# Kernel optimization log

Hardware: AMD Instinct MI355X
Metric: run time of the kernel (lower is better)

Reference implementation:

```python
import jax, jax.numpy as jnp
import numpy as np

X_GRID, Y_GRID = 192, 132
HW = X_GRID * Y_GRID            # 25344
NUM_PROP = 500
NUM_CLS = 6
RADIUS = 10
L_WIN = (2 * RADIUS + 1) ** 2   # 441
D = 128
N_HEADS = 8
D_HEAD = D // N_HEADS
VX, VY = 0.64, 0.64             # feature_map_stride * voxel_size
PC_X0, PC_Y0 = -61.44, -42.24


def _bev_pos():
    # create_2D_grid: linspace(0, size-1, size) + 0.5, meshgrid 'ij', flatten row-major
    bx, by = jnp.meshgrid(jnp.arange(X_GRID, dtype=jnp.float32) + 0.5,
                          jnp.arange(Y_GRID, dtype=jnp.float32) + 0.5, indexing='ij')
    return jnp.stack([bx.reshape(-1), by.reshape(-1)], axis=-1)[None]  # [1, HW, 2]


def conv2d(x, w, b):
    y = jax.lax.conv_general_dilated(x, w, (1, 1), 'SAME',
                                     dimension_numbers=('NCHW', 'OIHW', 'NCHW'))
    return y + b[None, :, None, None]


def maxpool3_valid(x):
    return jax.lax.reduce_window(x, -jnp.inf, jax.lax.max,
                                 (1, 1, 3, 3), (1, 1, 1, 1), 'VALID')


def layer_norm(x, g, b, eps=1e-5):
    m = jnp.mean(x, axis=-1, keepdims=True)
    v = jnp.var(x, axis=-1, keepdims=True)
    return (x - m) * jax.lax.rsqrt(v + eps) * g + b


def pos_emb(p, W1, b1, W2, b2):
    return jax.nn.relu(p @ W1 + b1) @ W2 + b2


def _forward(inputs, W_shared, b_shared, W_hm, b_hm, W_cls, b_cls,
             W_pos1, b_pos1, W_pos2, b_pos2, Wq, bq, Wk, bk, Wv, bv, Wo, bo,
             ln1_g, ln1_b, ln2_g, ln2_b, W_ff1, b_ff1, W_ff2, b_ff2,
             W_center, b_center, W_height, b_height, W_dim, b_dim,
             W_rot, b_rot, W_iou, b_iou, W_hm2, b_hm2):
    x = jnp.transpose(inputs, (0, 1, 3, 2))          # [B,C,192,132]
    B = x.shape[0]
    lidar_feat = jax.nn.relu(conv2d(x, W_shared, b_shared))   # [B,128,192,132]
    lff = lidar_feat.reshape(B, D, HW)

    dense_heatmap = conv2d(lidar_feat, W_hm, b_hm)            # [B,6,192,132]
    heatmap = jax.nn.sigmoid(jax.lax.stop_gradient(dense_heatmap))  # detached in original

    # local-max NMS: 3x3 maxpool on inner region, zeros at border; classes 3..5 bypass NMS
    inner = maxpool3_valid(heatmap)
    local_max = jnp.pad(inner, ((0, 0), (0, 0), (1, 1), (1, 1)))
    local_max = local_max.at[:, 3:6].set(heatmap[:, 3:6])
    hm = heatmap * (heatmap == local_max)

    # threshold + top-k proposals (replaces nonzero+pad+MySortImpe plugin)
    hm_flat = hm.reshape(B, NUM_CLS * HW)
    vals = jnp.where(hm_flat > 0.01, hm_flat, 0.0)
    _, top = jax.lax.top_k(vals, NUM_PROP)            # [B,500]
    cls = top // HW
    sp = top % HW

    query_feat = jnp.take_along_axis(lff, sp[:, None, :], axis=2)  # [B,128,500]
    oh = jax.nn.one_hot(cls, NUM_CLS, dtype=lff.dtype)             # [B,500,6]
    query_feat = query_feat + jnp.einsum('bpc,oc->bop', oh, W_cls) + b_cls[None, :, None]

    bev_pos = jnp.broadcast_to(_bev_pos(), (B, HW, 2))
    query_pos = jnp.take_along_axis(bev_pos, sp[:, :, None], axis=1)  # [B,500,2]

    # windowed key indices (faithful to original //x_grid, %y_grid arithmetic)
    rng = jnp.arange(-RADIUS, RADIUS + 1)
    rx, ry = jnp.meshgrid(rng, rng, indexing='ij')
    kx = (sp // X_GRID)[:, :, None, None] + rx[None, None]
    ky = (sp % Y_GRID)[:, :, None, None] + ry[None, None]
    key_idx = kx.reshape(B, NUM_PROP, L_WIN) * X_GRID + ky.reshape(B, NUM_PROP, L_WIN)
    key_mask = (key_idx < 0) | (key_idx >= HW)
    key_idx = jnp.clip(key_idx, 0, HW - 1)

    key_feat = jnp.take_along_axis(lff, key_idx.reshape(B, 1, -1), axis=2)
    key_feat = key_feat.reshape(B, D, NUM_PROP, L_WIN)
    key_pos = jnp.take_along_axis(bev_pos, key_idx.reshape(B, -1, 1), axis=1)
    key_pos = key_pos.reshape(B, NUM_PROP, L_WIN, 2)

    # decoder: cross-attention of each proposal over its 441-key window
    N = B * NUM_PROP
    q = query_feat.transpose(0, 2, 1).reshape(N, D)
    k = key_feat.transpose(0, 2, 3, 1).reshape(N, L_WIN, D)
    mask = key_mask.reshape(N, L_WIN)
    qpe = pos_emb(query_pos.reshape(N, 2), W_pos1, b_pos1, W_pos2, b_pos2)
    kpe = pos_emb(key_pos.reshape(N, L_WIN, 2), W_pos1, b_pos1, W_pos2, b_pos2)

    qh = ((q + qpe) @ Wq + bq).reshape(N, N_HEADS, D_HEAD)
    kh = ((k + kpe) @ Wk + bk).reshape(N, L_WIN, N_HEADS, D_HEAD)
    vh = (k @ Wv + bv).reshape(N, L_WIN, N_HEADS, D_HEAD)
    scores = jnp.einsum('nhd,nlhd->nhl', qh, kh) / np.float32(np.sqrt(D_HEAD))
    scores = jnp.where(mask[:, None, :], jnp.float32(-1e9), scores)
    attn = jax.nn.softmax(scores, axis=-1)
    ctx = jnp.einsum('nhl,nlhd->nhd', attn, vh).reshape(N, D)
    x1 = layer_norm(q + ctx @ Wo + bo, ln1_g, ln1_b)
    ff = jax.nn.relu(x1 @ W_ff1 + b_ff1) @ W_ff2 + b_ff2
    x2 = layer_norm(x1 + ff, ln2_g, ln2_b)

    qf = x2.reshape(B, NUM_PROP, D).transpose(0, 2, 1)   # [B,128,500]
    head = lambda W, b: jnp.einsum('bcp,oc->bop', qf, W) + b[None, :, None]
    center = head(W_center, b_center) + query_pos.transpose(0, 2, 1)
    height = head(W_height, b_height)
    dim = head(W_dim, b_dim)
    rot = head(W_rot, b_rot)
    iou = head(W_iou, b_iou)
    hm2 = head(W_hm2, b_hm2)

    # get_bboxes / decode_bbox
    score = jax.nn.sigmoid(hm2)                          # [B,6,500]
    _ = (iou + 1.0) * 0.5                                # computed, unused (as in original)
    final_preds = jnp.argmax(score, axis=1).astype(score.dtype)
    final_scores = jnp.max(score, axis=1)
    cx = center[:, 0:1] * VX + PC_X0
    cy = center[:, 1:2] * VY + PC_Y0
    dim = jnp.exp(dim)
    height = height - dim[:, 2:3] * 0.5
    rot = jnp.arctan(rot[:, 0:1] / (rot[:, 1:2] + 1e-6))
    box = jnp.concatenate([cx, cy, height, dim, rot,
                           final_preds[:, None, :], final_scores[:, None, :]], axis=1)
    return box.transpose(0, 2, 1)                        # [B,500,9]


def setup_inputs() -> dict:
    key = jax.random.key(0)
    ks = jax.random.split(key, 20)
    r = lambda k, shape, s=0.02: jax.random.normal(k, shape, dtype=jnp.float32) * s
    z = lambda n: jnp.zeros((n,), dtype=jnp.float32)
    o = lambda n: jnp.ones((n,), dtype=jnp.float32)
    return {
        'inputs': jax.random.normal(ks[0], (1, 256, 132, 192), dtype=jnp.float32),
        'W_shared': r(ks[1], (128, 256, 3, 3)), 'b_shared': z(128),
        'W_hm': r(ks[2], (6, 128, 3, 3)), 'b_hm': z(6),
        'W_cls': r(ks[3], (128, 6)), 'b_cls': z(128),
        'W_pos1': r(ks[4], (2, 128)), 'b_pos1': z(128),
        'W_pos2': r(ks[5], (128, 128)), 'b_pos2': z(128),
        'Wq': r(ks[6], (128, 128)), 'bq': z(128),
        'Wk': r(ks[7], (128, 128)), 'bk': z(128),
        'Wv': r(ks[8], (128, 128)), 'bv': z(128),
        'Wo': r(ks[9], (128, 128)), 'bo': z(128),
        'ln1_g': o(128), 'ln1_b': z(128),
        'ln2_g': o(128), 'ln2_b': z(128),
        'W_ff1': r(ks[10], (128, 256)), 'b_ff1': z(256),
        'W_ff2': r(ks[11], (256, 128)), 'b_ff2': z(128),
        'W_center': r(ks[12], (2, 128)), 'b_center': z(2),
        'W_height': r(ks[13], (1, 128)), 'b_height': z(1),
        'W_dim': r(ks[14], (3, 128)), 'b_dim': z(3),
        'W_rot': r(ks[15], (2, 128)), 'b_rot': z(2),
        'W_iou': r(ks[16], (1, 128)), 'b_iou': z(1),
        'W_hm2': r(ks[17], (6, 128)), 'b_hm2': z(6),
    }


def reference(inputs, W_shared, b_shared, W_hm, b_hm, W_cls, b_cls,
              W_pos1, b_pos1, W_pos2, b_pos2, Wq, bq, Wk, bk, Wv, bv, Wo, bo,
              ln1_g, ln1_b, ln2_g, ln2_b, W_ff1, b_ff1, W_ff2, b_ff2,
              W_center, b_center, W_height, b_height, W_dim, b_dim,
              W_rot, b_rot, W_iou, b_iou, W_hm2, b_hm2):
    return _forward(inputs, W_shared, b_shared, W_hm, b_hm, W_cls, b_cls,
                    W_pos1, b_pos1, W_pos2, b_pos2, Wq, bq, Wk, bk, Wv, bv, Wo, bo,
                    ln1_g, ln1_b, ln2_g, ln2_b, W_ff1, b_ff1, W_ff2, b_ff2,
                    W_center, b_center, W_height, b_height, W_dim, b_dim,
                    W_rot, b_rot, W_iou, b_iou, W_hm2, b_hm2)
```

## Files before the change

### kernel.cpp

```cpp
#include <hip/hip_runtime.h>
#include <math.h>
#include <float.h>

#define XG 192
#define YG 132
#define HW 25344
#define NCLS 6
#define NPROP 500
#define LWIN 441
#define CAP 2048

typedef unsigned short ushort_t;
typedef __attribute__((ext_vector_type(8))) short bf8v;
typedef __attribute__((ext_vector_type(4))) float f4v;

static __device__ __forceinline__ int imin(int a,int b){return a<b?a:b;}
static __device__ __forceinline__ int imax(int a,int b){return a>b?a:b;}

__device__ __forceinline__ void gl_lds16(const float* gp, float* lp){
  __builtin_amdgcn_global_load_lds(
      (const __attribute__((address_space(1))) unsigned int*)gp,
      (__attribute__((address_space(3))) unsigned int*)lp,
      16, 0, 0);
}
__device__ __forceinline__ void gl_lds16u(const ushort_t* gp, ushort_t* lp){
  __builtin_amdgcn_global_load_lds(
      (const __attribute__((address_space(1))) unsigned int*)gp,
      (__attribute__((address_space(3))) unsigned int*)lp,
      16, 0, 0);
}

__device__ __forceinline__ ushort_t f2bf(float x){
  unsigned u = __float_as_uint(x);
  return (ushort_t)((u + 0x7FFFu + ((u>>16)&1u)) >> 16);
}
__device__ __forceinline__ float bf2f(ushort_t h){
  return __uint_as_float(((unsigned)h)<<16);
}

__global__ __launch_bounds__(256) void k_wt(const float* __restrict__ Ws,
                                            const float* __restrict__ Whm,
                                            const float* __restrict__ Wq,
                                            const float* __restrict__ Wp2,
                                            const float* __restrict__ Wo,
                                            const float* __restrict__ Wf1,
                                            const float* __restrict__ Wf2,
                                            float* __restrict__ W6,
                                            float* __restrict__ WQT,
                                            float* __restrict__ WP2T,
                                            float* __restrict__ WOT,
                                            float* __restrict__ WF1T,
                                            float* __restrict__ WF2T,
                                            ushort_t* __restrict__ BQ0,
                                            ushort_t* __restrict__ BQ1,
                                            ushort_t* __restrict__ BQ2,
                                            int* __restrict__ Z){
  int t = blockIdx.x*256 + threadIdx.x;
  if (t < 294912){
    int kl = t & 31;
    int rest = t >> 5;
    int n = rest & 127;
    int tc = rest >> 7;
    int tap = tc >> 3, chunk = tc & 7;
    int c = chunk*32 + kl;
    float v = Ws[(size_t)n*2304 + c*9 + tap];
    ushort_t h0 = f2bf(v);
    float r1 = v - bf2f(h0);
    ushort_t h1 = f2bf(r1);
    float r2 = r1 - bf2f(h1);
    ushort_t h2 = f2bf(r2);
    size_t dst = (size_t)tc*5120 + n*40 + kl;
    BQ0[dst] = h0; BQ1[dst] = h1; BQ2[dst] = h2;
  }
  if (t < 6912){
    int c = t & 127, row = t >> 7;
    int cls = row / 9, tap = row % 9;
    W6[t] = Whm[(size_t)cls*1152 + c*9 + tap];
  }
  if (t < 16384){
    int k = t & 127, c = t >> 7;
    WQT[t]  = Wq [(size_t)k*128 + c];
    WP2T[t] = Wp2[(size_t)k*128 + c];
    WOT[t]  = Wo [(size_t)k*128 + c];
  }
  if (t < 32768){
    { int k = t & 127, o = t >> 7;  WF1T[t] = Wf1[(size_t)k*256 + o]; }
    { int k = t & 255, c = t >> 8;  WF2T[t] = Wf2[(size_t)k*128 + c]; }
  }
  if (t < 65568) Z[t] = 0;
}

__global__ __launch_bounds__(256, 3) void k_conv1(const float* __restrict__ IN,
                                                  const ushort_t* __restrict__ BQ0,
                                                  const ushort_t* __restrict__ BQ1,
                                                  const ushort_t* __restrict__ BQ2,
                                                  const float* __restrict__ bias,
                                                  float* __restrict__ LFF){
  const int b  = blockIdx.x;
  const int i0 = (b % 3) * 64;
  const int j  = b / 3;
  const int tid = threadIdx.x;
  const int w    = tid >> 6;
  const int lane = tid & 63;
  const int l15  = lane & 15, quad = lane >> 4;
  __shared__ __align__(16) ushort_t SM[23280];
  ushort_t* As0 = SM;
  ushort_t* As1 = SM + 2640;
  ushort_t* As2 = SM + 5280;
  ushort_t* Bs0 = SM + 7920;
  ushort_t* Bs1 = SM + 13040;
  ushort_t* Bs2 = SM + 18160;
  f4v acc[4][2];
  #pragma unroll
  for (int mq=0;mq<4;++mq)
    #pragma unroll
    for (int nt=0;nt<2;++nt) acc[mq][nt] = (f4v){0.f,0.f,0.f,0.f};

  for (int chunk=0; chunk<8; ++chunk){
    for (int kw=0; kw<3; ++kw){
      __syncthreads();
      {
        int gj = j - 1 + kw;
        bool jok = (unsigned)gj < 132u;
        for (int e = tid; e < 2112; e += 256){
          int c = e / 66, ii = e - c*66;
          int gi = i0 - 1 + ii;
          float v = 0.f;
          if (jok && (unsigned)gi < 192u)
            v = IN[(size_t)(chunk*32 + c)*25344 + gj*192 + gi];
          ushort_t h0 = f2bf(v);
          float r1 = v - bf2f(h0);
          ushort_t h1 = f2bf(r1);
          float r2 = r1 - bf2f(h1);
          ushort_t h2 = f2bf(r2);
          int a = ii*40 + c;
          As0[a] = h0; As1[a] = h1; As2[a] = h2;
        }
      }
      for (int kh=0; kh<3; ++kh){
        if (kh > 0) __syncthreads();
        {
          int tc = (kh*3 + kw)*8 + chunk;
          const ushort_t* s0 = BQ0 + (size_t)tc*5120;
          const ushort_t* s1 = BQ1 + (size_t)tc*5120;
          const ushort_t* s2 = BQ2 + (size_t)tc*5120;
          gl_lds16u(s0 + (size_t)tid*8,       Bs0 + (size_t)(w*64)*8);
          gl_lds16u(s0 + (size_t)(256+tid)*8, Bs0 + (size_t)(256 + w*64)*8);
          gl_lds16u(s1 + (size_t)tid*8,       Bs1 + (size_t)(w*64)*8);
          gl_lds16u(s1 + (size_t)(256+tid)*8, Bs1 + (size_t)(256 + w*64)*8);
          gl_lds16u(s2 + (size_t)tid*8,       Bs2 + (size_t)(w*64)*8);
          gl_lds16u(s2 + (size_t)(256+tid)*8, Bs2 + (size_t)(256 + w*64)*8);
          if (tid < 128){
            gl_lds16u(s0 + (size_t)(512+tid)*8, Bs0 + (size_t)(512 + w*64)*8);
            gl_lds16u(s1 + (size_t)(512+tid)*8, Bs1 + (size_t)(512 + w*64)*8);
            gl_lds16u(s2 + (size_t)(512+tid)*8, Bs2 + (size_t)(512 + w*64)*8);
          }
        }
        __syncthreads();
        bf8v A0[4], A1[4], A2[4];
        #pragma unroll
        for (int mq=0; mq<4; ++mq){
          int off = (mq*16 + l15 + kh)*40 + quad*8;
          A0[mq] = *(const bf8v*)&As0[off];
          A1[mq] = *(const bf8v*)&As1[off];
          A2[mq] = *(const bf8v*)&As2[off];
        }
        bf8v B0[2], B1[2], B2[2];
        #pragma unroll
        for (int ntl=0; ntl<2; ++ntl){
          int off = ((w*2+ntl)*16 + l15)*40 + quad*8;
          B0[ntl] = *(const bf8v*)&Bs0[off];
          B1[ntl] = *(const bf8v*)&Bs1[off];
          B2[ntl] = *(const bf8v*)&Bs2[off];
        }
        #pragma unroll
        for (int mq=0;mq<4;++mq){
          #pragma unroll
          for (int ntl=0;ntl<2;++ntl){
            f4v c = acc[mq][ntl];
            c = __builtin_amdgcn_mfma_f32_16x16x32_bf16(A0[mq], B0[ntl], c, 0,0,0);
            c = __builtin_amdgcn_mfma_f32_16x16x32_bf16(A0[mq], B1[ntl], c, 0,0,0);
            c = __builtin_amdgcn_mfma_f32_16x16x32_bf16(A1[mq], B0[ntl], c, 0,0,0);
            c = __builtin_amdgcn_mfma_f32_16x16x32_bf16(A0[mq], B2[ntl], c, 0,0,0);
            c = __builtin_amdgcn_mfma_f32_16x16x32_bf16(A1[mq], B1[ntl], c, 0,0,0);
            c = __builtin_amdgcn_mfma_f32_16x16x32_bf16(A2[mq], B0[ntl], c, 0,0,0);
            acc[mq][ntl] = c;
          }
        }
      }
    }
  }
  __syncthreads();
  float* Cs = (float*)SM;
  #pragma unroll
  for (int mq=0;mq<4;++mq)
    #pragma unroll
    for (int ntl=0;ntl<2;++ntl)
      #pragma unroll
      for (int r=0;r<4;++r){
        int m = mq*16 + quad*4 + r;
        int oc = (w*2+ntl)*16 + l15;
        Cs[m*128 + oc] = acc[mq][ntl][r];
      }
  __syncthreads();
  for (int e = tid; e < 2048; e += 256){
    int m = e >> 5, ocq = e & 31;
    float4 v = *(float4*)&Cs[m*128 + ocq*4];
    float4 bs = *(const float4*)&bias[ocq*4];
    v.x = fmaxf(v.x + bs.x, 0.f);
    v.y = fmaxf(v.y + bs.y, 0.f);
    v.z = fmaxf(v.z + bs.z, 0.f);
    v.w = fmaxf(v.w + bs.w, 0.f);
    int p = (i0 + m)*132 + j;
    *(float4*)&LFF[(size_t)p*128 + ocq*4] = v;
  }
}

__global__ __launch_bounds__(256) void k_mid(const float* __restrict__ LFF,
                                             const float* __restrict__ W1, const float* __restrict__ b1,
                                             const float* __restrict__ W2, const float* __restrict__ b2,
                                             const float* __restrict__ Wk, const float* __restrict__ bk,
                                             const float* __restrict__ Wv, const float* __restrict__ bv,
                                             float* __restrict__ KK, float* __restrict__ VV,
                                             const float* __restrict__ W6, const float* __restrict__ bhm,
                                             float* __restrict__ HMS){
  __shared__ float smem[12288];
  const int tid = threadIdx.x;
  const int wv4 = tid >> 6;
  if (blockIdx.x < 792){
    float* hs   = smem;
    float* sf   = smem + 4096;
    float* wbuf = smem + 8192;
    const int p0 = blockIdx.x*32;
    for (int e=tid; e<4096; e+=256){
      int k = e>>5, px = e&31;
      int p = p0+px;
      float bx = (float)(p/132)+0.5f, by = (float)(p%132)+0.5f;
      hs[k*32+px] = fmaxf(bx*W1[k] + by*W1[128+k] + b1[k], 0.f);
    }
    for (int e=tid; e<4096; e+=256){
      int px = e>>7, k = e&127;
      sf[k*32+px] = LFF[(size_t)(p0+px)*128 + k];
    }
    const int pxg = tid & 15, ocg = tid >> 4;
    const int px0 = pxg*2, oc0 = ocg*8;
    float accA[2][8];
    #pragma unroll
    for (int r=0;r<2;++r)
      #pragma unroll
      for (int u=0;u<8;++u) accA[r][u]=0.f;
    for (int c0=0; c0<128; c0+=32){
      __syncthreads();
      const float* wsrc = W2 + (size_t)c0*128;
      #pragma unroll
      for (int r=0;r<4;++r)
        gl_lds16(wsrc + (size_t)(r*256+tid)*4, wbuf + (size_t)(r*256+wv4*64)*4);
      __syncthreads();
      #pragma unroll 2
      for (int k=0;k<32;++k){
        float a0 = hs[(c0+k)*32+px0], a1 = hs[(c0+k)*32+px0+1];
        const float4* w = (const float4*)(wbuf + (size_t)k*128 + oc0);
        float4 w0 = w[0], w1 = w[1];
        accA[0][0]+=a0*w0.x; accA[0][1]+=a0*w0.y; accA[0][2]+=a0*w0.z; accA[0][3]+=a0*w0.w;
        accA[0][4]+=a0*w1.x; accA[0][5]+=a0*w1.y; accA[0][6]+=a0*w1.z; accA[0][7]+=a0*w1.w;
        accA[1][0]+=a1*w0.x; accA[1][1]+=a1*w0.y; accA[1][2]+=a1*w0.z; accA[1][3]+=a1*w0.w;
        accA[1][4]+=a1*w1.x; accA[1][5]+=a1*w1.y; accA[1][6]+=a1*w1.z; accA[1][7]+=a1*w1.w;
      }
    }
    __syncthreads();
    #pragma unroll
    for (int u=0;u<8;++u){
      float bb = b2[oc0+u];
      hs[(oc0+u)*32+px0]   = sf[(oc0+u)*32+px0]   + accA[0][u] + bb;
      hs[(oc0+u)*32+px0+1] = sf[(oc0+u)*32+px0+1] + accA[1][u] + bb;
    }
    float accK[2][8], accV[2][8];
    #pragma unroll
    for (int u=0;u<8;++u){
      float k0 = bk[oc0+u], v0 = bv[oc0+u];
      accK[0][u]=k0; accK[1][u]=k0; accV[0][u]=v0; accV[1][u]=v0;
    }
    for (int c0=0; c0<128; c0+=16){
      __syncthreads();
      #pragma unroll
      for (int r=0;r<2;++r){
        gl_lds16(Wk + (size_t)c0*128 + (size_t)(r*256+tid)*4, wbuf + (size_t)(r*256+wv4*64)*4);
        gl_lds16(Wv + (size_t)c0*128 + (size_t)(r*256+tid)*4, wbuf + 2048 + (size_t)(r*256+wv4*64)*4);
      }
      __syncthreads();
      #pragma unroll 2
      for (int k=0;k<16;++k){
        int kk = c0+k;
        float s0 = hs[kk*32+px0], s1 = hs[kk*32+px0+1];
        float f0 = sf[kk*32+px0], f1 = sf[kk*32+px0+1];
        const float4* wkp = (const float4*)(wbuf + (size_t)k*128 + oc0);
        const float4* wvp = (const float4*)(wbuf + 2048 + (size_t)k*128 + oc0);
        float4 k0v = wkp[0], k1v = wkp[1], v0v = wvp[0], v1v = wvp[1];
        accK[0][0]+=s0*k0v.x; accK[0][1]+=s0*k0v.y; accK[0][2]+=s0*k0v.z; accK[0][3]+=s0*k0v.w;
        accK[0][4]+=s0*k1v.x; accK[0][5]+=s0*k1v.y; accK[0][6]+=s0*k1v.z; accK[0][7]+=s0*k1v.w;
        accK[1][0]+=s1*k0v.x; accK[1][1]+=s1*k0v.y; accK[1][2]+=s1*k0v.z; accK[1][3]+=s1*k0v.w;
        accK[1][4]+=s1*k1v.x; accK[1][5]+=s1*k1v.y; accK[1][6]+=s1*k1v.z; accK[1][7]+=s1*k1v.w;
        accV[0][0]+=f0*v0v.x; accV[0][1]+=f0*v0v.y; accV[0][2]+=f0*v0v.z; accV[0][3]+=f0*v0v.w;
        accV[0][4]+=f0*v1v.x; accV[0][5]+=f0*v1v.y; accV[0][6]+=f0*v1v.z; accV[0][7]+=f0*v1v.w;
        accV[1][0]+=f1*v0v.x; accV[1][1]+=f1*v0v.y; accV[1][2]+=f1*v0v.z; accV[1][3]+=f1*v0v.w;
        accV[1][4]+=f1*v1v.x; accV[1][5]+=f1*v1v.y; accV[1][6]+=f1*v1v.z; accV[1][7]+=f1*v1v.w;
      }
    }
    #pragma unroll
    for (int r=0;r<2;++r){
      int p = p0+px0+r;
      float4* oK = (float4*)(KK + (size_t)p*128 + oc0);
      float4* oV = (float4*)(VV + (size_t)p*128 + oc0);
      float4 t0, t1;
      t0.x=accK[r][0]; t0.y=accK[r][1]; t0.z=accK[r][2]; t0.w=accK[r][3];
      t1.x=accK[r][4]; t1.y=accK[r][5]; t1.z=accK[r][6]; t1.w=accK[r][7];
      oK[0]=t0; oK[1]=t1;
      t0.x=accV[r][0]; t0.y=accV[r][1]; t0.z=accV[r][2]; t0.w=accV[r][3];
      t1.x=accV[r][4]; t1.y=accV[r][5]; t1.z=accV[r][6]; t1.w=accV[r][7];
      oV[0]=t0; oV[1]=t1;
    }
  } else {
    float* w6s = smem;
    float* red = smem + 8192;
    for (int e=tid; e<6912; e+=256) w6s[e] = W6[e];
    __syncthreads();
    int lane = tid & 63, wave = tid >> 6;
    int p = (blockIdx.x - 792)*64 + lane;
    int i = p/132, j = p%132;
    float acc[6] = {0.f,0.f,0.f,0.f,0.f,0.f};
    int cbase = wave*32;
    #pragma unroll
    for (int kh=0; kh<3; ++kh){
      int gi = i+kh-1;
      if ((unsigned)gi >= 192u) continue;
      #pragma unroll
      for (int kw=0; kw<3; ++kw){
        int gj = j+kw-1;
        if ((unsigned)gj >= 132u) continue;
        const float* row = LFF + (size_t)(gi*132+gj)*128 + cbase;
        int tap = kh*3+kw;
        #pragma unroll
        for (int cq=0; cq<8; ++cq){
          float4 v = *(const float4*)(row + cq*4);
          #pragma unroll
          for (int cls=0; cls<6; ++cls){
            float4 wv = *(const float4*)(w6s + (size_t)(cls*9+tap)*128 + cbase + cq*4);
            acc[cls] += v.x*wv.x + v.y*wv.y + v.z*wv.z + v.w*wv.w;
          }
        }
      }
    }
    __syncthreads();
    #pragma unroll
    for (int c=0;c<6;++c) red[(wave*6+c)*64 + lane] = acc[c];
    __syncthreads();
    if (wave==0){
      #pragma unroll
      for (int c=0;c<6;++c){
        float s = red[c*64+lane] + red[(6+c)*64+lane] + red[(12+c)*64+lane] + red[(18+c)*64+lane] + bhm[c];
        HMS[(size_t)c*HW + p] = 1.f/(1.f+expf(-s));
      }
    }
  }
}

__global__ __launch_bounds__(256) void k_nms(const float* __restrict__ HMS,
                                             float* __restrict__ VALS,
                                             int* __restrict__ HIST){
  int t = blockIdx.x*256 + threadIdx.x;
  int c = t / HW, p = t % HW;
  int i = p/132, j = p%132;
  float h = HMS[t];
  float v;
  if (c < 3){
    v = 0.f;
    if (i>=1 && i<=190 && j>=1 && j<=130){
      float m = -1e30f;
      #pragma unroll
      for (int di=-1;di<=1;++di)
        #pragma unroll
        for (int dj=-1;dj<=1;++dj)
          m = fmaxf(m, HMS[(size_t)c*HW + (i+di)*132 + (j+dj)]);
      if (h == m) v = h;
    }
  } else v = h;
  if (!(v > 0.01f)) v = 0.f;
  VALS[t] = v;
  if (v > 0.f) atomicAdd(HIST + (__float_as_uint(v)>>16), 1);
}

__global__ __launch_bounds__(1024) void k_scan(const int* __restrict__ HIST, int* __restrict__ SCAN){
  __shared__ int part[1024];
  __shared__ int gsel;
  int t = threadIdx.x;
  int s = 0, base = t*64;
  for (int u=0;u<64;++u) s += HIST[base+u];
  part[t] = s;
  __syncthreads();
  for (int off=1; off<1024; off<<=1){
    int add = (t+off < 1024) ? part[t+off] : 0;
    __syncthreads();
    part[t] += add;
    __syncthreads();
  }
  int total = part[0];
  int mineI = part[t];
  int nextI = (t < 1023) ? part[t+1] : 0;
  if (mineI >= NPROP && nextI < NPROP) gsel = t;
  if (t == 0 && total < NPROP) gsel = -1;
  __syncthreads();
  int g = gsel;
  if (g < 0){
    if (t==0){ SCAN[0] = 0; SCAN[1] = total; }
    return;
  }
  int cumG = (g < 1023) ? part[g+1] : 0;
  if (t < 64){
    int x = HIST[g*64 + t];
    #pragma unroll
    for (int off=1; off<64; off<<=1){
      int y = __shfl_down(x, off);
      x += (t + off < 64) ? y : 0;
    }
    int Snext = __shfl_down(x, 1);
    int incl  = cumG + x;
    int nextc = (t==63) ? cumG : cumG + Snext;
    if (incl >= NPROP && nextc < NPROP){
      SCAN[0] = g*64 + t;
      SCAN[1] = nextc;
    }
  }
}

__global__ __launch_bounds__(256) void k_collect(const float* __restrict__ VALS,
                                                 const int* __restrict__ SCAN,
                                                 int* __restrict__ CNT,
                                                 float* __restrict__ CV, int* __restrict__ CI){
  int t = blockIdx.x*256 + threadIdx.x;
  float v = VALS[t];
  int bstar = SCAN[0];
  if (v > 0.f && (int)(__float_as_uint(v)>>16) >= bstar){
    int pos = atomicAdd(CNT, 1);
    if (pos < CAP){ CV[pos] = v; CI[pos] = t; }
  }
}

__global__ __launch_bounds__(1024) void k_sort(const float* __restrict__ CV, const int* __restrict__ CI,
                                               const int* __restrict__ CNT,
                                               int* __restrict__ TOPS, int* __restrict__ TOPC){
  __shared__ float sv[CAP];
  __shared__ int   si[CAP];
  int tid = threadIdx.x;
  int M = imin(CNT[0], CAP);
  for (int i=tid; i<CAP; i+=1024){
    if (i < M){ sv[i] = CV[i]; si[i] = CI[i]; }
    else      { sv[i] = -1.f;  si[i] = 0x7fffffff; }
  }
  __syncthreads();
  for (int k=2; k<=CAP; k<<=1){
    for (int j=k>>1; j>0; j>>=1){
      for (int i=tid; i<CAP; i+=1024){
        int p = i ^ j;
        if (p > i){
          bool up = ((i & k) == 0);
          float va = sv[i], vb = sv[p];
          int ia = si[i], ib = si[p];
          bool aFirst = (va > vb) || (va == vb && ia < ib);
          bool bFirst = (vb > va) || (vb == va && ib < ia);
          bool doswap = up ? bFirst : aFirst;
          if (doswap){ sv[i]=vb; sv[p]=va; si[i]=ib; si[p]=ia; }
        }
      }
      __syncthreads();
    }
  }
  for (int t=tid; t<NPROP; t+=1024){
    int idx = imin(si[t], NCLS*HW - 1);
    TOPC[t] = idx / HW;
    TOPS[t] = idx % HW;
  }
}

__global__ __launch_bounds__(256) void k_attn(const float* __restrict__ KK, const float* __restrict__ VV,
                                              const float* __restrict__ LFF,
                                              const int* __restrict__ TOPS, const int* __restrict__ TOPC,
                                              const float* __restrict__ Wcls, const float* __restrict__ bcls,
                                              const float* __restrict__ pW1, const float* __restrict__ pb1,
                                              const float* __restrict__ WP2T, const float* __restrict__ pb2,
                                              const float* __restrict__ WQT, const float* __restrict__ bq,
                                              const float* __restrict__ WOT, const float* __restrict__ bo,
                                              const float* __restrict__ g1, const float* __restrict__ b1,
                                              const float* __restrict__ WF1T, const float* __restrict__ bf1,
                                              const float* __restrict__ WF2T, const float* __restrict__ bf2,
                                              const float* __restrict__ g2, const float* __restrict__ b2,
                                              const float* __restrict__ Wc, const float* __restrict__ bc,
                                              const float* __restrict__ Wh, const float* __restrict__ bh,
                                              const float* __restrict__ Wd, const float* __restrict__ bd,
                                              const float* __restrict__ Wr, const float* __restrict__ br,
                                              const float* __restrict__ Whm2, const float* __restrict__ bhm2,
                                              float* __restrict__ out){
  int n = blockIdx.x, tid = threadIdx.x;
  __shared__ __align__(16) float qhL[128];
  __shared__ float sc[8*441];
  __shared__ int   kiL[441];
  __shared__ __align__(16) float ctxL[128];
  __shared__ float xL[128];
  __shared__ float hidL[256];
  __shared__ float sumsL[8];
  __shared__ float stat[2];
  __shared__ float dots[16];
  int sp = TOPS[n];
  int cls = TOPC[n];
  const int kb64 = (tid>>7)*64, c128 = tid&127;
  float qreg = 0.f;
  if (tid < 128){
    float qx = (float)(sp/132)+0.5f, qy = (float)(sp%132)+0.5f;
    ctxL[tid] = fmaxf(qx*pW1[tid] + qy*pW1[128+tid] + pb1[tid], 0.f);
    qreg = LFF[(size_t)sp*128+tid] + Wcls[tid*6+cls] + bcls[tid];
  }
  __syncthreads();
  {
    const float4* wp = (const float4*)(WP2T + (size_t)c128*128 + kb64);
    float pe = 0.f;
    #pragma unroll
    for (int k4=0;k4<16;++k4){
      float4 w = wp[k4]; int kb = kb64 + k4*4;
      pe += ctxL[kb]*w.x + ctxL[kb+1]*w.y + ctxL[kb+2]*w.z + ctxL[kb+3]*w.w;
    }
    sc[tid] = pe;
  }
  __syncthreads();
  if (tid < 128) xL[tid] = qreg + pb2[tid] + sc[tid] + sc[tid+128];
  __syncthreads();
  {
    const float4* wp = (const float4*)(WQT + (size_t)c128*128 + kb64);
    float qh = 0.f;
    #pragma unroll
    for (int k4=0;k4<16;++k4){
      float4 w = wp[k4]; int kb = kb64 + k4*4;
      qh += xL[kb]*w.x + xL[kb+1]*w.y + xL[kb+2]*w.z + xL[kb+3]*w.w;
    }
    sc[tid] = qh;
  }
  __syncthreads();
  if (tid < 128) qhL[tid] = bq[tid] + sc[tid] + sc[tid+128];
  __syncthreads();
  int spx = sp/192, spy = sp%132;
  for (int l = tid; l < 441; l += 256){
    int a = l/21, bb = l%21;
    int kidx = (spx + a - 10)*192 + (spy + bb - 10);
    bool msk = (kidx < 0) || (kidx >= HW);
    int kc = imin(imax(kidx,0), HW-1);
    kiL[l] = kc;
    const float4* kk4 = (const float4*)(KK + (size_t)kc*128);
    const float4* qh4 = (const float4*)qhL;
    #pragma unroll
    for (int hh=0; hh<8; ++hh){
      float acc = 0.f;
      #pragma unroll
      for (int d4=0; d4<4; ++d4){
        float4 kv = kk4[hh*4+d4]; float4 qv = qh4[hh*4+d4];
        acc += kv.x*qv.x + kv.y*qv.y + kv.z*qv.z + kv.w*qv.w;
      }
      sc[hh*441+l] = msk ? -1e9f : acc*0.25f;
    }
  }
  __syncthreads();
  int wave = tid>>6, lane = tid&63;
  for (int hh = wave; hh < 8; hh += 4){
    float mx = -3.0e38f;
    for (int l = lane; l < 441; l += 64) mx = fmaxf(mx, sc[hh*441+l]);
    #pragma unroll
    for (int off=32; off; off>>=1) mx = fmaxf(mx, __shfl_xor(mx, off));
    float sum = 0.f;
    for (int l = lane; l < 441; l += 64){
      float e = __expf(sc[hh*441+l] - mx);
      sc[hh*441+l] = e; sum += e;
    }
    #pragma unroll
    for (int off=32; off; off>>=1) sum += __shfl_xor(sum, off);
    if (lane==0) sumsL[hh] = sum;
  }
  __syncthreads();
  for (int hh = wave; hh < 8; hh += 4){
    float a[16];
    #pragma unroll
    for (int d=0; d<16; ++d) a[d]=0.f;
    for (int l = lane; l < 441; l += 64){
      float w = sc[hh*441+l];
      const float4* vv4 = (const float4*)(VV + (size_t)kiL[l]*128 + hh*16);
      #pragma unroll
      for (int d4=0; d4<4; ++d4){
        float4 v = vv4[d4];
        a[d4*4+0]+=w*v.x; a[d4*4+1]+=w*v.y; a[d4*4+2]+=w*v.z; a[d4*4+3]+=w*v.w;
      }
    }
    #pragma unroll
    for (int d=0; d<16; ++d){
      #pragma unroll
      for (int off=32; off; off>>=1) a[d] += __shfl_xor(a[d], off);
    }
    if (lane==0){
      float inv = 1.f/sumsL[hh];
      #pragma unroll
      for (int d=0; d<16; ++d) ctxL[hh*16+d] = a[d]*inv;
    }
  }
  __syncthreads();
  {
    const float4* wp = (const float4*)(WOT + (size_t)c128*128 + kb64);
    float acc = 0.f;
    #pragma unroll
    for (int k4=0;k4<16;++k4){
      float4 w = wp[k4]; int kb = kb64 + k4*4;
      acc += ctxL[kb]*w.x + ctxL[kb+1]*w.y + ctxL[kb+2]*w.z + ctxL[kb+3]*w.w;
    }
    sc[tid] = acc;
  }
  __syncthreads();
  float x1v = 0.f;
  if (tid < 128){
    x1v = qreg + bo[tid] + sc[tid] + sc[tid+128];
    xL[tid] = x1v;
  }
  __syncthreads();
  if (tid < 64){
    float u0 = xL[tid], u1 = xL[tid+64];
    float s = u0+u1, s2 = u0*u0+u1*u1;
    #pragma unroll
    for (int off=32; off; off>>=1){ s += __shfl_xor(s, off); s2 += __shfl_xor(s2, off); }
    if (tid==0){ float mean = s*(1.f/128.f); float var = s2*(1.f/128.f) - mean*mean;
      stat[0]=mean; stat[1]=rsqrtf(var + 1e-5f); }
  }
  __syncthreads();
  if (tid < 128) xL[tid] = (x1v - stat[0])*stat[1]*g1[tid] + b1[tid];
  __syncthreads();
  {
    const float4* wp = (const float4*)(WF1T + (size_t)tid*128);
    float hv = bf1[tid];
    #pragma unroll 8
    for (int k4=0;k4<32;++k4){
      float4 w = wp[k4]; int kb = k4*4;
      hv += xL[kb]*w.x + xL[kb+1]*w.y + xL[kb+2]*w.z + xL[kb+3]*w.w;
    }
    hidL[tid] = fmaxf(hv, 0.f);
  }
  __syncthreads();
  {
    int kb0 = (tid>>7)*128;
    const float4* wp = (const float4*)(WF2T + (size_t)c128*256 + kb0);
    float acc = 0.f;
    #pragma unroll 8
    for (int k4=0;k4<32;++k4){
      float4 w = wp[k4]; int kb = kb0 + k4*4;
      acc += hidL[kb]*w.x + hidL[kb+1]*w.y + hidL[kb+2]*w.z + hidL[kb+3]*w.w;
    }
    sc[tid] = acc;
  }
  __syncthreads();
  float x2v = 0.f;
  if (tid < 128) x2v = xL[tid] + bf2[tid] + sc[tid] + sc[tid+128];
  __syncthreads();
  if (tid < 128) hidL[tid] = x2v;
  __syncthreads();
  if (tid < 64){
    float u0 = hidL[tid], u1 = hidL[tid+64];
    float s = u0+u1, s2 = u0*u0+u1*u1;
    #pragma unroll
    for (int off=32; off; off>>=1){ s += __shfl_xor(s, off); s2 += __shfl_xor(s2, off); }
    if (tid==0){ float mean = s*(1.f/128.f); float var = s2*(1.f/128.f) - mean*mean;
      stat[0]=mean; stat[1]=rsqrtf(var + 1e-5f); }
  }
  __syncthreads();
  if (tid < 128) xL[tid] = (x2v - stat[0])*stat[1]*g2[tid] + b2[tid];
  __syncthreads();
  if (tid < 14){
    const float* Wp; float bb;
    if (tid < 2)      { Wp = Wc + tid*128;        bb = bc[tid];      }
    else if (tid < 3) { Wp = Wh;                  bb = bh[0];        }
    else if (tid < 6) { Wp = Wd + (tid-3)*128;    bb = bd[tid-3];    }
    else if (tid < 8) { Wp = Wr + (tid-6)*128;    bb = br[tid-6];    }
    else              { Wp = Whm2 + (tid-8)*128;  bb = bhm2[tid-8];  }
    float acc = bb;
    for (int k=0;k<128;++k) acc += xL[k]*Wp[k];
    dots[tid] = acc;
  }
  __syncthreads();
  if (tid == 0){
    float qpx = (float)(sp/132)+0.5f, qpy = (float)(sp%132)+0.5f;
    float cx = (dots[0]+qpx)*0.64f - 61.44f;
    float cy = (dots[1]+qpy)*0.64f - 42.24f;
    float e0 = expf(dots[3]), e1 = expf(dots[4]), e2 = expf(dots[5]);
    float hgt = dots[2] - e2*0.5f;
    float rot = atanf(dots[6]/(dots[7] + 1e-6f));
    float bestv = -1.f; int bestc = 0;
    #pragma unroll
    for (int m=0;m<6;++m){
      float s = 1.f/(1.f + expf(-dots[8+m]));
      if (s > bestv){ bestv = s; bestc = m; }
    }
    float* o = out + (size_t)n*9;
    o[0]=cx; o[1]=cy; o[2]=hgt; o[3]=e0; o[4]=e1; o[5]=e2; o[6]=rot;
    o[7]=(float)bestc; o[8]=bestv;
  }
}

extern "C" void kernel_launch(void* const* d_in, const int* in_sizes, int n_in,
                              void* d_out, int out_size, void* d_ws, size_t ws_size,
                              hipStream_t stream){
  (void)in_sizes; (void)n_in; (void)out_size;
  const float* IN   = (const float*)d_in[0];
  const float* Wsh  = (const float*)d_in[1];
  const float* bsh  = (const float*)d_in[2];
  const float* Whm  = (const float*)d_in[3];
  const float* bhm  = (const float*)d_in[4];
  const float* Wcls = (const float*)d_in[5];
  const float* bcls = (const float*)d_in[6];
  const float* Wp1  = (const float*)d_in[7];
  const float* bp1  = (const float*)d_in[8];
  const float* Wp2  = (const float*)d_in[9];
  const float* bp2  = (const float*)d_in[10];
  const float* Wq   = (const float*)d_in[11];
  const float* bq   = (const float*)d_in[12];
  const float* Wk   = (const float*)d_in[13];
  const float* bk   = (const float*)d_in[14];
  const float* Wv   = (const float*)d_in[15];
  const float* bv   = (const float*)d_in[16];
  const float* Wo   = (const float*)d_in[17];
  const float* bo   = (const float*)d_in[18];
  const float* g1   = (const float*)d_in[19];
  const float* b1   = (const float*)d_in[20];
  const float* g2   = (const float*)d_in[21];
  const float* b2   = (const float*)d_in[22];
  const float* Wf1  = (const float*)d_in[23];
  const float* bf1  = (const float*)d_in[24];
  const float* Wf2  = (const float*)d_in[25];
  const float* bf2  = (const float*)d_in[26];
  const float* Wc   = (const float*)d_in[27];
  const float* bc   = (const float*)d_in[28];
  const float* Wh   = (const float*)d_in[29];
  const float* bh   = (const float*)d_in[30];
  const float* Wd   = (const float*)d_in[31];
  const float* bd   = (const float*)d_in[32];
  const float* Wr   = (const float*)d_in[33];
  const float* br   = (const float*)d_in[34];
  const float* Whm2 = (const float*)d_in[37];
  const float* bhm2 = (const float*)d_in[38];
  float* out = (float*)d_out;
  float* W = (float*)d_ws;

  const size_t N_LFF  = (size_t)HW*128;
  const size_t OFF_LFF  = 0;
  const size_t OFF_KK   = OFF_LFF + N_LFF;
  const size_t OFF_VV   = OFF_KK + N_LFF;
  const size_t OFF_W6   = OFF_VV + N_LFF;
  const size_t OFF_HMS  = OFF_W6 + 6912;
  const size_t OFF_VALS = OFF_HMS + 152064;
  const size_t OFF_HIST = OFF_VALS + 152064;
  const size_t OFF_SCAN = OFF_HIST + 65536;
  const size_t OFF_CNT  = OFF_SCAN + 16;
  const size_t OFF_CV   = OFF_CNT + 16;
  const size_t OFF_CI   = OFF_CV + CAP;
  const size_t OFF_TOPS = OFF_CI + CAP;
  const size_t OFF_TOPC = OFF_TOPS + 512;
  const size_t OFF_WQT  = OFF_TOPC + 512;
  const size_t OFF_WP2T = OFF_WQT + 16384;
  const size_t OFF_WOT  = OFF_WP2T + 16384;
  const size_t OFF_WF1T = OFF_WOT + 16384;
  const size_t OFF_WF2T = OFF_WF1T + 32768;
  const size_t OFF_BQ0  = OFF_WF2T + 32768;
  const size_t OFF_BQ1  = OFF_BQ0 + 184320;
  const size_t OFF_BQ2  = OFF_BQ1 + 184320;
  const size_t TOTAL    = OFF_BQ2 + 184320;
  if (ws_size < TOTAL*sizeof(float)) return;

  ushort_t* BQ0 = (ushort_t*)(W + OFF_BQ0);
  ushort_t* BQ1 = (ushort_t*)(W + OFF_BQ1);
  ushort_t* BQ2 = (ushort_t*)(W + OFF_BQ2);

  k_wt    <<<1152, 256, 0, stream>>>(Wsh, Whm, Wq, Wp2, Wo, Wf1, Wf2,
                                     W+OFF_W6,
                                     W+OFF_WQT, W+OFF_WP2T, W+OFF_WOT, W+OFF_WF1T, W+OFF_WF2T,
                                     BQ0, BQ1, BQ2,
                                     (int*)(W+OFF_HIST));
  k_conv1 <<<396, 256, 0, stream>>>(IN, BQ0, BQ1, BQ2, bsh, W+OFF_LFF);
  k_mid   <<<1188, 256, 0, stream>>>(W+OFF_LFF, Wp1, bp1, Wp2, bp2, Wk, bk, Wv, bv,
                                     W+OFF_KK, W+OFF_VV, W+OFF_W6, bhm, W+OFF_HMS);
  k_nms   <<<594,  256, 0, stream>>>(W+OFF_HMS, W+OFF_VALS, (int*)(W+OFF_HIST));
  k_scan  <<<1,   1024, 0, stream>>>((const int*)(W+OFF_HIST), (int*)(W+OFF_SCAN));
  k_collect<<<594, 256, 0, stream>>>(W+OFF_VALS, (const int*)(W+OFF_SCAN),
                                     (int*)(W+OFF_CNT), W+OFF_CV, (int*)(W+OFF_CI));
  k_sort  <<<1,   1024, 0, stream>>>(W+OFF_CV, (const int*)(W+OFF_CI), (const int*)(W+OFF_CNT),
                                     (int*)(W+OFF_TOPS), (int*)(W+OFF_TOPC));
  k_attn  <<<500,  256, 0, stream>>>(W+OFF_KK, W+OFF_VV, W+OFF_LFF,
                                     (const int*)(W+OFF_TOPS), (const int*)(W+OFF_TOPC),
                                     Wcls, bcls, Wp1, bp1, W+OFF_WP2T, bp2, W+OFF_WQT, bq,
                                     W+OFF_WOT, bo, g1, b1, W+OFF_WF1T, bf1, W+OFF_WF2T, bf2, g2, b2,
                                     Wc, bc, Wh, bh, Wd, bd, Wr, br, Whm2, bhm2, out);
}
```

Measured before the change: 543.1 us.

## Split conv1 input channels across two grid slices with a reduction kernel

The shared 3x3 conv now runs with a second grid dimension, so each slice handles half of the input-channel chunks and writes partial sums into the KK and VV scratch buffers. A new elementwise kernel adds the two partials, applies bias and ReLU, and writes LFF. This doubles the block count from 396 to 792 to fill more CUs on the GPU. In exchange it adds a kernel launch and extra global traffic: two partial writes plus a read-back of about 13 MB each way.

New measurement: 541.7 us, median of 2. Within noise of the previous version (-0.3%).

```diff
diff --git a/kernel.cpp b/kernel.cpp
--- a/kernel.cpp
+++ b/kernel.cpp
@@ -94,9 +94,10 @@
                                                   const ushort_t* __restrict__ BQ0,
                                                   const ushort_t* __restrict__ BQ1,
                                                   const ushort_t* __restrict__ BQ2,
-                                                  const float* __restrict__ bias,
-                                                  float* __restrict__ LFF){
+                                                  float* __restrict__ P0,
+                                                  float* __restrict__ P1){
   const int b  = blockIdx.x;
+  const int g  = blockIdx.y;
   const int i0 = (b % 3) * 64;
   const int j  = b / 3;
   const int tid = threadIdx.x;
@@ -116,7 +117,8 @@
     #pragma unroll
     for (int nt=0;nt<2;++nt) acc[mq][nt] = (f4v){0.f,0.f,0.f,0.f};
 
-  for (int chunk=0; chunk<8; ++chunk){
+  for (int cq=0; cq<4; ++cq){
+    const int chunk = g*4 + cq;
     for (int kw=0; kw<3; ++kw){
       __syncthreads();
       {
@@ -203,17 +205,29 @@
         Cs[m*128 + oc] = acc[mq][ntl][r];
       }
   __syncthreads();
+  float* dst = g ? P1 : P0;
   for (int e = tid; e < 2048; e += 256){
     int m = e >> 5, ocq = e & 31;
     float4 v = *(float4*)&Cs[m*128 + ocq*4];
-    float4 bs = *(const float4*)&bias[ocq*4];
-    v.x = fmaxf(v.x + bs.x, 0.f);
-    v.y = fmaxf(v.y + bs.y, 0.f);
-    v.z = fmaxf(v.z + bs.z, 0.f);
-    v.w = fmaxf(v.w + bs.w, 0.f);
     int p = (i0 + m)*132 + j;
-    *(float4*)&LFF[(size_t)p*128 + ocq*4] = v;
-  }
+    *(float4*)&dst[(size_t)p*128 + ocq*4] = v;
+  }
+}
+
+__global__ __launch_bounds__(256) void k_cadd2(float* __restrict__ LFF,
+                                               const float* __restrict__ P0,
+                                               const float* __restrict__ P1,
+                                               const float* __restrict__ bias){
+  int t = blockIdx.x*256 + threadIdx.x;
+  float4 a = ((const float4*)P0)[t];
+  float4 b = ((const float4*)P1)[t];
+  float4 bs = ((const float4*)bias)[t & 31];
+  float4 r;
+  r.x = fmaxf(a.x+b.x+bs.x, 0.f);
+  r.y = fmaxf(a.y+b.y+bs.y, 0.f);
+  r.z = fmaxf(a.z+b.z+bs.z, 0.f);
+  r.w = fmaxf(a.w+b.w+bs.w, 0.f);
+  ((float4*)LFF)[t] = r;
 }
 
 __global__ __launch_bounds__(256) void k_mid(const float* __restrict__ LFF,
@@ -783,7 +797,8 @@
                                      W+OFF_WQT, W+OFF_WP2T, W+OFF_WOT, W+OFF_WF1T, W+OFF_WF2T,
                                      BQ0, BQ1, BQ2,
                                      (int*)(W+OFF_HIST));
-  k_conv1 <<<396, 256, 0, stream>>>(IN, BQ0, BQ1, BQ2, bsh, W+OFF_LFF);
+  k_conv1 <<<dim3(396,2), 256, 0, stream>>>(IN, BQ0, BQ1, BQ2, W+OFF_KK, W+OFF_VV);
+  k_cadd2 <<<3168, 256, 0, stream>>>(W+OFF_LFF, W+OFF_KK, W+OFF_VV, bsh);
   k_mid   <<<1188, 256, 0, stream>>>(W+OFF_LFF, Wp1, bp1, Wp2, bp2, Wk, bk, Wv, bv,
                                      W+OFF_KK, W+OFF_VV, W+OFF_W6, bhm, W+OFF_HMS);
   k_nms   <<<594,  256, 0, stream>>>(W+OFF_HMS, W+OFF_VALS, (int*)(W+OFF_HIST));
```
